# Optimization experiments

Hardware: AMD Instinct MI355X
Metric: run time of the kernel (lower is better)

## Reference

```python
import jax, jax.numpy as jnp
import numpy as np

B, S, E = 2, 2048, 1024
H, KV, D = 16, 4, 64
GC = 128          # ve_gate_channels
EPS = 1.1920929e-07  # torch F.rms_norm default eps for fp32
NEG = -1e30


def setup_inputs() -> dict:
    key = jax.random.key(0)
    ks = jax.random.split(key, 8)
    x = jax.random.normal(ks[0], (B, S, E), jnp.float32)
    ve = jax.random.normal(ks[1], (B, S, KV * D), jnp.float32)
    half = D // 2
    inv_freq = 1.0 / (10000.0 ** (np.arange(half, dtype=np.float64) / half))
    ang = np.arange(S, dtype=np.float64)[:, None] * inv_freq[None, :]
    cos = jnp.asarray(np.cos(ang), jnp.float32)[:, None, :]  # [S,1,D/2]
    sin = jnp.asarray(np.sin(ang), jnp.float32)[:, None, :]
    sc = E ** -0.5
    Wq = jax.random.normal(ks[2], (E, H * D), jnp.float32) * sc
    Wk = jax.random.normal(ks[3], (E, KV * D), jnp.float32) * sc
    Wv = jax.random.normal(ks[4], (E, KV * D), jnp.float32) * sc
    Wproj = jax.random.normal(ks[5], (E, E), jnp.float32) * sc
    Wgate = jax.random.normal(ks[6], (GC, KV), jnp.float32) * (GC ** -0.5)
    return {"x": x, "ve": ve, "cos": cos, "sin": sin, "Wq": Wq, "Wk": Wk,
            "Wv": Wv, "Wproj": Wproj, "Wgate": Wgate,
            "window_left": 1024, "window_right": 0}


def _rms(x):
    return x * jax.lax.rsqrt(jnp.mean(x * x, axis=-1, keepdims=True) + EPS)


def _rope(x, cos, sin):
    d = x.shape[-1] // 2
    x1, x2 = x[..., :d], x[..., d:]
    return jnp.concatenate([x1 * cos + x2 * sin, -x1 * sin + x2 * cos], axis=-1)


def reference(x, ve, cos, sin, Wq, Wk, Wv, Wproj, Wgate, window_left, window_right):
    b, s, e = x.shape
    q = (x @ Wq).reshape(b, s, H, D)
    k = (x @ Wk).reshape(b, s, KV, D)
    v = (x @ Wv).reshape(b, s, KV, D)
    # value-embedding gate: 2*sigmoid over first GC channels, per kv-head
    gate = 2.0 * jax.nn.sigmoid(x[..., :GC] @ Wgate)          # [B,S,KV]
    v = v + gate[..., None] * ve.reshape(b, s, KV, D)
    q = _rms(_rope(q, cos, sin))
    k = _rms(_rope(k, cos, sin))
    # GQA: repeat kv heads to match query heads
    g = H // KV
    kk = jnp.repeat(k, g, axis=2)                             # [B,S,H,D]
    vv = jnp.repeat(v, g, axis=2)
    scores = jnp.einsum('bihd,bjhd->bhij', q, kk) * (D ** -0.5)
    i = jnp.arange(s)[:, None]
    j = jnp.arange(s)[None, :]
    mask = (j <= i + window_right) & (j >= i - window_left) & (j <= i)
    scores = jnp.where(mask, scores, NEG)
    p = jax.nn.softmax(scores, axis=-1)
    y = jnp.einsum('bhij,bjhd->bihd', p, vv).reshape(b, s, H * D)
    return y @ Wproj
```

## Files before the change

kernel.cpp:

```cpp
#include <hip/hip_runtime.h>

typedef __bf16 bf16;
typedef __bf16 bf16x4 __attribute__((ext_vector_type(4)));
typedef __bf16 bf16x8 __attribute__((ext_vector_type(8)));
typedef float floatx4 __attribute__((ext_vector_type(4)));

#define EPS 1.1920929e-07f
#define QSCALE (0.125f * 1.44269504088896f)
#define SHIFT_C 11.5416f

__device__ __forceinline__ floatx4 mfma16(bf16x8 a, bf16x8 b, floatx4 c) {
  return __builtin_amdgcn_mfma_f32_16x16x32_bf16(a, b, c, 0, 0, 0);
}

__device__ __forceinline__ void gload16(const void* g, void* l) {
  __builtin_amdgcn_global_load_lds((const __attribute__((address_space(1))) unsigned int*)g,
                                   (__attribute__((address_space(3))) unsigned int*)l, 16, 0, 0);
}

__global__ void prep_kernel(const float* __restrict__ x, const float* __restrict__ wgate,
                            const float* __restrict__ Wq, const float* __restrict__ Wk,
                            const float* __restrict__ Wv, const float* __restrict__ Wproj,
                            bf16* __restrict__ xb, float* __restrict__ gate,
                            bf16* __restrict__ out_qkv, bf16* __restrict__ out_proj) {
  __shared__ float tile[32][33];
  const int tid = threadIdx.x;
  if (blockIdx.x < 4096) {
    int t = blockIdx.x;
    const float* xr = x + (size_t)t * 1024;
    float4 v = *(const float4*)(xr + tid * 4);
    bf16x4 o = {(bf16)v.x, (bf16)v.y, (bf16)v.z, (bf16)v.w};
    *(bf16x4*)(xb + (size_t)t * 1024 + tid * 4) = o;
    if (tid < 64) {
      int c = (tid & 31) * 4;
#pragma unroll
      for (int kv = 0; kv < 4; kv++) {
        float g = v.x * wgate[(c + 0) * 4 + kv] + v.y * wgate[(c + 1) * 4 + kv] +
                  v.z * wgate[(c + 2) * 4 + kv] + v.w * wgate[(c + 3) * 4 + kv];
        g += __shfl_xor(g, 1, 64);
        g += __shfl_xor(g, 2, 64);
        g += __shfl_xor(g, 4, 64);
        g += __shfl_xor(g, 8, 64);
        g += __shfl_xor(g, 16, 64);
        if (tid == 0) {
          int b = t >> 11, s = t & 2047;
          gate[((size_t)b * 4 + kv) * 2048 + s] = 2.f / (1.f + __expf(-g));
        }
      }
    }
  } else {
    int j = blockIdx.x - 4096;
    int ky = j / 80;
    int nx = j - ky * 80;
    int k0 = ky * 32;
    int tx = tid & 31, ty = tid >> 5;
    if (nx < 48) {
      int n0 = nx * 32;
#pragma unroll
      for (int i = 0; i < 4; i++) {
        int k = k0 + ty + i * 8, n = n0 + tx;
        float v;
        if (n < 1024)      v = Wq[(size_t)k * 1024 + n];
        else if (n < 1280) v = Wk[(size_t)k * 256 + (n - 1024)];
        else               v = Wv[(size_t)k * 256 + (n - 1280)];
        tile[ty + i * 8][tx] = v;
      }
      __syncthreads();
#pragma unroll
      for (int i = 0; i < 4; i++) {
        int n = n0 + ty + i * 8, k = k0 + tx;
        out_qkv[(size_t)n * 1024 + k] = (bf16)tile[tx][ty + i * 8];
      }
    } else {
      int n0 = (nx - 48) * 32;
#pragma unroll
      for (int i = 0; i < 4; i++)
        tile[ty + i * 8][tx] = Wproj[(size_t)(k0 + ty + i * 8) * 1024 + n0 + tx];
      __syncthreads();
#pragma unroll
      for (int i = 0; i < 4; i++)
        out_proj[(size_t)(n0 + ty + i * 8) * 1024 + k0 + tx] = (bf16)tile[tx][ty + i * 8];
    }
  }
}

__global__ __launch_bounds__(256) void qkv_gemm_kernel(const bf16* __restrict__ A,
                                                       const bf16* __restrict__ Bt,
                                                       const float* __restrict__ ve,
                                                       const float* __restrict__ cosb,
                                                       const float* __restrict__ sinb,
                                                       const float* __restrict__ gate,
                                                       bf16* __restrict__ Qb,
                                                       bf16* __restrict__ Kf,
                                                       bf16* __restrict__ Vf) {
  __shared__ __align__(16) char smem[24576];
  bf16* As = (bf16*)smem;
  bf16* Bs = (bf16*)(smem + 16384);
  bf16* Ep = (bf16*)smem;
  const int K = 1024;
  const int tid = threadIdx.x;
  const int orig = blockIdx.x;
  const int lid = (orig & 7) * 96 + (orig >> 3);
  const int tile = lid % 24;
  const int m0 = (lid / 24) * 128, n0 = tile * 64;
  const int w = tid >> 6, lane = tid & 63;
  const int q = lane >> 4, r0 = lane & 15;
  const int lrow = lane >> 2, lcol = (lane & 3) * 8;
  const int b = m0 >> 11, s0 = m0 & 2047;

  floatx4 acc[2][4];
#pragma unroll
  for (int i = 0; i < 2; i++)
#pragma unroll
    for (int j = 0; j < 4; j++) acc[i][j] = (floatx4){0.f, 0.f, 0.f, 0.f};

  for (int k0 = 0; k0 < K; k0 += 64) {
    __syncthreads();
#pragma unroll
    for (int i = 0; i < 4; i++) {
      int g = w * 4 + i, s = g >> 3, rb = g & 7;
      gload16(A + (size_t)(m0 + rb * 16 + lrow) * K + k0 + s * 32 + lcol, &As[s * 4096 + rb * 512]);
    }
#pragma unroll
    for (int i = 0; i < 2; i++) {
      int g = w * 2 + i, s = g >> 2, rb = g & 3;
      gload16(Bt + (size_t)(n0 + rb * 16 + lrow) * K + k0 + s * 32 + lcol, &Bs[s * 2048 + rb * 512]);
    }
    __syncthreads();
#pragma unroll
    for (int s = 0; s < 2; s++) {
      bf16x8 af[2], bfr[4];
#pragma unroll
      for (int mt = 0; mt < 2; mt++) af[mt] = *(const bf16x8*)&As[s * 4096 + (w * 32 + mt * 16 + r0) * 32 + q * 8];
#pragma unroll
      for (int nt = 0; nt < 4; nt++) bfr[nt] = *(const bf16x8*)&Bs[s * 2048 + (nt * 16 + r0) * 32 + q * 8];
#pragma unroll
      for (int mt = 0; mt < 2; mt++)
#pragma unroll
        for (int nt = 0; nt < 4; nt++)
          acc[mt][nt] = mfma16(af[mt], bfr[nt], acc[mt][nt]);
    }
  }
  __syncthreads();

  if (tile < 16) {
    const int h = tile;
#pragma unroll
    for (int mt = 0; mt < 2; mt++) {
      float rvv[4][4];
#pragma unroll
      for (int ntp = 0; ntp < 2; ntp++) {
        int d31 = ntp * 16 + r0;
#pragma unroll
        for (int r = 0; r < 4; r++) {
          int s = s0 + w * 32 + mt * 16 + q * 4 + r;
          float c = cosb[s * 32 + d31], sn = sinb[s * 32 + d31];
          float v1 = acc[mt][ntp][r], v2 = acc[mt][ntp + 2][r];
          rvv[ntp][r] = v1 * c + v2 * sn;
          rvv[ntp + 2][r] = v2 * c - v1 * sn;
        }
      }
#pragma unroll
      for (int r = 0; r < 4; r++) {
        float ss = 0.f;
#pragma unroll
        for (int nt = 0; nt < 4; nt++) ss += rvv[nt][r] * rvv[nt][r];
        ss += __shfl_xor(ss, 1, 64);
        ss += __shfl_xor(ss, 2, 64);
        ss += __shfl_xor(ss, 4, 64);
        ss += __shfl_xor(ss, 8, 64);
        float sc = rsqrtf(ss * (1.f / 64.f) + EPS) * QSCALE;
        int row = w * 32 + mt * 16 + q * 4 + r;
#pragma unroll
        for (int nt = 0; nt < 4; nt++)
          Ep[row * 72 + nt * 16 + r0] = (bf16)(rvv[nt][r] * sc);
      }
    }
    __syncthreads();
#pragma unroll
    for (int p = 0; p < 4; p++) {
      int g = p * 256 + tid;
      int row = g >> 3, chunk = g & 7;
      *(uint4*)&Qb[(((size_t)b * 16 + h) * 2048 + s0 + row) * 64 + chunk * 8] =
          *(const uint4*)&Ep[row * 72 + chunk * 8];
    }
  } else if (tile < 20) {
    const int kv = tile - 16;
#pragma unroll
    for (int mt = 0; mt < 2; mt++) {
      float rvv[4][4];
#pragma unroll
      for (int ntp = 0; ntp < 2; ntp++) {
        int d31 = ntp * 16 + r0;
#pragma unroll
        for (int r = 0; r < 4; r++) {
          int s = s0 + w * 32 + mt * 16 + q * 4 + r;
          float c = cosb[s * 32 + d31], sn = sinb[s * 32 + d31];
          float v1 = acc[mt][ntp][r], v2 = acc[mt][ntp + 2][r];
          rvv[ntp][r] = v1 * c + v2 * sn;
          rvv[ntp + 2][r] = v2 * c - v1 * sn;
        }
      }
#pragma unroll
      for (int r = 0; r < 4; r++) {
        float ss = 0.f;
#pragma unroll
        for (int nt = 0; nt < 4; nt++) ss += rvv[nt][r] * rvv[nt][r];
        ss += __shfl_xor(ss, 1, 64);
        ss += __shfl_xor(ss, 2, 64);
        ss += __shfl_xor(ss, 4, 64);
        ss += __shfl_xor(ss, 8, 64);
        float sc = rsqrtf(ss * (1.f / 64.f) + EPS);
        int row = w * 32 + mt * 16 + q * 4 + r;
#pragma unroll
        for (int nt = 0; nt < 4; nt++)
          Ep[row * 72 + nt * 16 + r0] = (bf16)(rvv[nt][r] * sc);
      }
    }
    __syncthreads();
    {
      int tk = (s0 >> 5) + w;
      size_t tb = ((size_t)(b * 4 + kv) * 64 + tk) * 2048;
#pragma unroll
      for (int u = 0; u < 4; u++) {
        int joff = (u >= 2) ? 16 : 0, doff = (u & 1) * 32;
        bf16x8 f = *(const bf16x8*)&Ep[(w * 32 + joff + r0) * 72 + doff + q * 8];
        *(bf16x8*)&Kf[tb + u * 512 + lane * 8] = f;
      }
    }
  } else {
    const int kv = tile - 20;
    const float* gbase = gate + ((size_t)b * 4 + kv) * 2048;
#pragma unroll
    for (int mt = 0; mt < 2; mt++) {
#pragma unroll
      for (int r = 0; r < 4; r++) {
        int row = w * 32 + mt * 16 + q * 4 + r;
        float gg = gbase[s0 + row];
#pragma unroll
        for (int nt = 0; nt < 4; nt++) {
          int d = nt * 16 + r0;
          float vv = acc[mt][nt][r] + gg * ve[(size_t)(m0 + row) * 256 + kv * 64 + d];
          Ep[row * 72 + d] = (bf16)vv;
        }
      }
    }
    __syncthreads();
    {
      int tk = (s0 >> 5) + w;
      size_t tb = ((size_t)(b * 4 + kv) * 64 + tk) * 2048;
#pragma unroll
      for (int nt = 0; nt < 4; nt++) {
        bf16 tmp[8];
#pragma unroll
        for (int e = 0; e < 8; e++) {
          int jl = w * 32 + (e >> 2) * 16 + 4 * q + (e & 3);
          tmp[e] = Ep[jl * 72 + nt * 16 + r0];
        }
        *(uint4*)&Vf[tb + nt * 512 + lane * 8] = *(uint4*)tmp;
      }
    }
  }
}

__global__ __launch_bounds__(256) void proj_gemm_kernel(const bf16* __restrict__ A,
                                                        const bf16* __restrict__ Bt,
                                                        float* __restrict__ Cout) {
  __shared__ __align__(16) bf16 As[2 * 128 * 32];
  __shared__ __align__(16) bf16 Bs[2 * 64 * 32];
  const int K = 1024, N = 1024;
  const int tid = threadIdx.x;
  const int orig = blockIdx.x;
  const int lid = (orig & 7) * 64 + (orig >> 3);
  const int m0 = (lid / 16) * 128, n0 = (lid % 16) * 64;
  const int w = tid >> 6, lane = tid & 63;
  const int q = lane >> 4, r0 = lane & 15;
  const int lrow = lane >> 2, lcol = (lane & 3) * 8;

  floatx4 acc[2][4];
#pragma unroll
  for (int i = 0; i < 2; i++)
#pragma unroll
    for (int j = 0; j < 4; j++) acc[i][j] = (floatx4){0.f, 0.f, 0.f, 0.f};

  for (int k0 = 0; k0 < K; k0 += 64) {
    __syncthreads();
#pragma unroll
    for (int i = 0; i < 4; i++) {
      int g = w * 4 + i, s = g >> 3, rb = g & 7;
      gload16(A + (size_t)(m0 + rb * 16 + lrow) * K + k0 + s * 32 + lcol, &As[s * 4096 + rb * 512]);
    }
#pragma unroll
    for (int i = 0; i < 2; i++) {
      int g = w * 2 + i, s = g >> 2, rb = g & 3;
      gload16(Bt + (size_t)(n0 + rb * 16 + lrow) * K + k0 + s * 32 + lcol, &Bs[s * 2048 + rb * 512]);
    }
    __syncthreads();
#pragma unroll
    for (int s = 0; s < 2; s++) {
      bf16x8 af[2], bfr[4];
#pragma unroll
      for (int mt = 0; mt < 2; mt++) af[mt] = *(const bf16x8*)&As[s * 4096 + (w * 32 + mt * 16 + r0) * 32 + q * 8];
#pragma unroll
      for (int nt = 0; nt < 4; nt++) bfr[nt] = *(const bf16x8*)&Bs[s * 2048 + (nt * 16 + r0) * 32 + q * 8];
#pragma unroll
      for (int mt = 0; mt < 2; mt++)
#pragma unroll
        for (int nt = 0; nt < 4; nt++)
          acc[mt][nt] = mfma16(af[mt], bfr[nt], acc[mt][nt]);
    }
  }
#pragma unroll
  for (int mt = 0; mt < 2; mt++)
#pragma unroll
    for (int nt = 0; nt < 4; nt++)
#pragma unroll
      for (int r = 0; r < 4; r++) {
        int row = m0 + w * 32 + mt * 16 + q * 4 + r;
        int col = n0 + nt * 16 + r0;
        Cout[(size_t)row * N + col] = acc[mt][nt][r];
      }
}

__global__ __launch_bounds__(256, 4) void attn_kernel(const bf16* __restrict__ Qb,
                                                      const bf16* __restrict__ Kf,
                                                      const bf16* __restrict__ Vf,
                                                      const int* __restrict__ wlp,
                                                      const int* __restrict__ wrp,
                                                      bf16* __restrict__ Yb) {
  __shared__ __align__(16) bf16 Ks[2048];
  __shared__ __align__(16) bf16 Vs[2048];
  const int wl = wlp[0];
  const int wrc = min(wrp[0], 0);
  const int blk = blockIdx.x;
  const int bkv = blk & 7;
  const int b = bkv >> 2, kvh = bkv & 3;
  const int cm = 127 - (blk >> 3);
  const int w = threadIdx.x >> 6, lane = threadIdx.x & 63;
  const int q = lane >> 4, r0 = lane & 15;
  const int h = kvh * 4 + w;
  const int q0 = cm << 4;

  const bf16* qbase = Qb + (((size_t)b * 16 + h) * 2048 + q0 + r0) * 64;
  bf16x8 aq0 = *(const bf16x8*)(qbase + q * 8);
  bf16x8 aq1 = *(const bf16x8*)(qbase + 32 + q * 8);

  floatx4 O[4];
#pragma unroll
  for (int nt = 0; nt < 4; nt++) O[nt] = (floatx4){0.f, 0.f, 0.f, 0.f};
  floatx4 L = (floatx4){0.f, 0.f, 0.f, 0.f};

  const bf16 onev = (bf16)1.0f;
  const bf16x8 ones = {onev, onev, onev, onev, onev, onev, onev, onev};

  const int jlo = max(0, q0 - wl) & ~31;
  const int jhi = q0 + 15 + wrc;
  const int count = ((jhi - jlo) >> 5) + 1;
  const int tile0 = jlo >> 5;

  const bf16* kfb = Kf + ((size_t)(b * 4 + kvh) * 64) * 2048;
  const bf16* vfb = Vf + ((size_t)(b * 4 + kvh) * 64) * 2048;

  for (int t = 0; t < count; t++) {
    const int j0 = jlo + (t << 5);
    const bf16* kt = kfb + (size_t)(tile0 + t) * 2048;
    const bf16* vt = vfb + (size_t)(tile0 + t) * 2048;
    __syncthreads();
#pragma unroll
    for (int i = 0; i < 2; i++) {
      int c = 2 * w + i;
      if (c < 4) gload16(kt + c * 512 + lane * 8, &Ks[c * 512]);
      else       gload16(vt + (c - 4) * 512 + lane * 8, &Vs[(c - 4) * 512]);
    }
    __syncthreads();

    bf16x8 kf0 = *(const bf16x8*)&Ks[0 * 512 + lane * 8];
    bf16x8 kf1 = *(const bf16x8*)&Ks[1 * 512 + lane * 8];
    bf16x8 kf2 = *(const bf16x8*)&Ks[2 * 512 + lane * 8];
    bf16x8 kf3 = *(const bf16x8*)&Ks[3 * 512 + lane * 8];

    floatx4 s0 = (floatx4){-SHIFT_C, -SHIFT_C, -SHIFT_C, -SHIFT_C};
    floatx4 s1 = s0;
    __builtin_amdgcn_s_setprio(1);
    s0 = mfma16(kf0, aq0, s0);
    s0 = mfma16(kf1, aq1, s0);
    s1 = mfma16(kf2, aq0, s1);
    s1 = mfma16(kf3, aq1, s1);
    __builtin_amdgcn_s_setprio(0);

    bf16x8 pa;
    if (j0 >= q0 + 15 - wl && j0 + 31 <= q0 + wrc) {
#pragma unroll
      for (int r = 0; r < 4; r++) {
        pa[r] = (bf16)exp2f(s0[r]);
        pa[4 + r] = (bf16)exp2f(s1[r]);
      }
    } else {
      const int i = q0 + r0;
#pragma unroll
      for (int r = 0; r < 4; r++) {
        int ja = j0 + 4 * q + r, jb = ja + 16;
        bool va = (ja <= i + wrc) && (ja >= i - wl);
        bool vb = (jb <= i + wrc) && (jb >= i - wl);
        pa[r] = va ? (bf16)exp2f(s0[r]) : (bf16)0.f;
        pa[4 + r] = vb ? (bf16)exp2f(s1[r]) : (bf16)0.f;
      }
    }

    bf16x8 vf0 = *(const bf16x8*)&Vs[0 * 512 + lane * 8];
    bf16x8 vf1 = *(const bf16x8*)&Vs[1 * 512 + lane * 8];
    bf16x8 vf2 = *(const bf16x8*)&Vs[2 * 512 + lane * 8];
    bf16x8 vf3 = *(const bf16x8*)&Vs[3 * 512 + lane * 8];

    __builtin_amdgcn_s_setprio(1);
    L = mfma16(pa, ones, L);
    O[0] = mfma16(pa, vf0, O[0]);
    O[1] = mfma16(pa, vf1, O[1]);
    O[2] = mfma16(pa, vf2, O[2]);
    O[3] = mfma16(pa, vf3, O[3]);
    __builtin_amdgcn_s_setprio(0);
  }

  float inv[4];
#pragma unroll
  for (int r = 0; r < 4; r++) inv[r] = 1.f / L[r];
#pragma unroll
  for (int nt = 0; nt < 4; nt++)
#pragma unroll
    for (int r = 0; r < 4; r++) {
      int i = q0 + q * 4 + r;
      Yb[((size_t)b * 2048 + i) * 1024 + h * 64 + nt * 16 + r0] = (bf16)(O[nt][r] * inv[r]);
    }
}

extern "C" void kernel_launch(void* const* d_in, const int* in_sizes, int n_in,
                              void* d_out, int out_size, void* d_ws, size_t ws_size,
                              hipStream_t stream) {
  const float* x     = (const float*)d_in[0];
  const float* ve    = (const float*)d_in[1];
  const float* cosb  = (const float*)d_in[2];
  const float* sinb  = (const float*)d_in[3];
  const float* Wq    = (const float*)d_in[4];
  const float* Wk    = (const float*)d_in[5];
  const float* Wv    = (const float*)d_in[6];
  const float* Wproj = (const float*)d_in[7];
  const float* Wgate = (const float*)d_in[8];
  const int* wl      = (const int*)d_in[9];
  const int* wr      = (const int*)d_in[10];

  char* ws = (char*)d_ws;
  bf16* Xb      = (bf16*)(ws);
  bf16* Wqkv_t  = (bf16*)(ws + 8388608);
  bf16* Wproj_t = (bf16*)(ws + 11534336);
  bf16* Qb      = (bf16*)(ws + 13631488);
  bf16* Kf      = (bf16*)(ws + 22020096);
  bf16* Vf      = (bf16*)(ws + 24117248);
  bf16* Yb      = (bf16*)(ws + 26214400);
  float* gateb  = (float*)(ws + 34603008);

  prep_kernel<<<4096 + 2560, 256, 0, stream>>>(x, Wgate, Wq, Wk, Wv, Wproj, Xb, gateb, Wqkv_t, Wproj_t);
  qkv_gemm_kernel<<<768, 256, 0, stream>>>(Xb, Wqkv_t, ve, cosb, sinb, gateb, Qb, Kf, Vf);
  attn_kernel<<<1024, 256, 0, stream>>>(Qb, Kf, Vf, wl, wr, Yb);
  proj_gemm_kernel<<<512, 256, 0, stream>>>(Yb, Wproj_t, (float*)d_out);
}
```

Before: 163.3 us.

## Process two 16-row query tiles per attention block to reuse K/V tiles

Each attention block now handles 32 query rows (two 16-row sub-tiles) instead of 16, so every K/V tile loaded into shared memory feeds twice as many MFMAs. The grid is halved to 512 blocks and the occupancy hint is dropped from launch_bounds. The aim is to cut global/LDS load traffic and barrier overhead per unit of work. The cost is more registers per thread and fewer blocks, which can lower occupancy and latency hiding. Each block also walks one extra key tile at the diagonal.

```diff
diff --git a/kernel.cpp b/kernel.cpp
--- a/kernel.cpp
+++ b/kernel.cpp
@@ -322,12 +322,12 @@
       }
 }
 
-__global__ __launch_bounds__(256, 4) void attn_kernel(const bf16* __restrict__ Qb,
-                                                      const bf16* __restrict__ Kf,
-                                                      const bf16* __restrict__ Vf,
-                                                      const int* __restrict__ wlp,
-                                                      const int* __restrict__ wrp,
-                                                      bf16* __restrict__ Yb) {
+__global__ __launch_bounds__(256) void attn_kernel(const bf16* __restrict__ Qb,
+                                                   const bf16* __restrict__ Kf,
+                                                   const bf16* __restrict__ Vf,
+                                                   const int* __restrict__ wlp,
+                                                   const int* __restrict__ wrp,
+                                                   bf16* __restrict__ Yb) {
   __shared__ __align__(16) bf16 Ks[2048];
   __shared__ __align__(16) bf16 Vs[2048];
   const int wl = wlp[0];
@@ -335,26 +335,33 @@
   const int blk = blockIdx.x;
   const int bkv = blk & 7;
   const int b = bkv >> 2, kvh = bkv & 3;
-  const int cm = 127 - (blk >> 3);
+  const int cm = 63 - (blk >> 3);
   const int w = threadIdx.x >> 6, lane = threadIdx.x & 63;
   const int q = lane >> 4, r0 = lane & 15;
   const int h = kvh * 4 + w;
-  const int q0 = cm << 4;
-
-  const bf16* qbase = Qb + (((size_t)b * 16 + h) * 2048 + q0 + r0) * 64;
-  bf16x8 aq0 = *(const bf16x8*)(qbase + q * 8);
-  bf16x8 aq1 = *(const bf16x8*)(qbase + 32 + q * 8);
-
-  floatx4 O[4];
-#pragma unroll
-  for (int nt = 0; nt < 4; nt++) O[nt] = (floatx4){0.f, 0.f, 0.f, 0.f};
-  floatx4 L = (floatx4){0.f, 0.f, 0.f, 0.f};
+  const int q0 = cm << 5;
+  const int qA = q0, qB = q0 + 16;
+
+  const bf16* qbase = Qb + (((size_t)b * 16 + h) * 2048 + qA + r0) * 64;
+  bf16x8 aqA0 = *(const bf16x8*)(qbase + q * 8);
+  bf16x8 aqA1 = *(const bf16x8*)(qbase + 32 + q * 8);
+  bf16x8 aqB0 = *(const bf16x8*)(qbase + 16 * 64 + q * 8);
+  bf16x8 aqB1 = *(const bf16x8*)(qbase + 16 * 64 + 32 + q * 8);
+
+  floatx4 OA[4], OB[4];
+#pragma unroll
+  for (int nt = 0; nt < 4; nt++) {
+    OA[nt] = (floatx4){0.f, 0.f, 0.f, 0.f};
+    OB[nt] = (floatx4){0.f, 0.f, 0.f, 0.f};
+  }
+  floatx4 LA = (floatx4){0.f, 0.f, 0.f, 0.f};
+  floatx4 LB = LA;
 
   const bf16 onev = (bf16)1.0f;
   const bf16x8 ones = {onev, onev, onev, onev, onev, onev, onev, onev};
 
   const int jlo = max(0, q0 - wl) & ~31;
-  const int jhi = q0 + 15 + wrc;
+  const int jhi = q0 + 31 + wrc;
   const int count = ((jhi - jlo) >> 5) + 1;
   const int tile0 = jlo >> 5;
 
@@ -379,31 +386,52 @@
     bf16x8 kf2 = *(const bf16x8*)&Ks[2 * 512 + lane * 8];
     bf16x8 kf3 = *(const bf16x8*)&Ks[3 * 512 + lane * 8];
 
-    floatx4 s0 = (floatx4){-SHIFT_C, -SHIFT_C, -SHIFT_C, -SHIFT_C};
-    floatx4 s1 = s0;
+    floatx4 sA0 = (floatx4){-SHIFT_C, -SHIFT_C, -SHIFT_C, -SHIFT_C};
+    floatx4 sA1 = sA0, sB0 = sA0, sB1 = sA0;
     __builtin_amdgcn_s_setprio(1);
-    s0 = mfma16(kf0, aq0, s0);
-    s0 = mfma16(kf1, aq1, s0);
-    s1 = mfma16(kf2, aq0, s1);
-    s1 = mfma16(kf3, aq1, s1);
+    sA0 = mfma16(kf0, aqA0, sA0);
+    sA0 = mfma16(kf1, aqA1, sA0);
+    sA1 = mfma16(kf2, aqA0, sA1);
+    sA1 = mfma16(kf3, aqA1, sA1);
+    sB0 = mfma16(kf0, aqB0, sB0);
+    sB0 = mfma16(kf1, aqB1, sB0);
+    sB1 = mfma16(kf2, aqB0, sB1);
+    sB1 = mfma16(kf3, aqB1, sB1);
     __builtin_amdgcn_s_setprio(0);
 
-    bf16x8 pa;
-    if (j0 >= q0 + 15 - wl && j0 + 31 <= q0 + wrc) {
-#pragma unroll
-      for (int r = 0; r < 4; r++) {
-        pa[r] = (bf16)exp2f(s0[r]);
-        pa[4 + r] = (bf16)exp2f(s1[r]);
+    bf16x8 paA, paB;
+    if (j0 >= qA + 15 - wl && j0 + 31 <= qA + wrc) {
+#pragma unroll
+      for (int r = 0; r < 4; r++) {
+        paA[r] = (bf16)exp2f(sA0[r]);
+        paA[4 + r] = (bf16)exp2f(sA1[r]);
       }
     } else {
-      const int i = q0 + r0;
+      const int i = qA + r0;
 #pragma unroll
       for (int r = 0; r < 4; r++) {
         int ja = j0 + 4 * q + r, jb = ja + 16;
         bool va = (ja <= i + wrc) && (ja >= i - wl);
         bool vb = (jb <= i + wrc) && (jb >= i - wl);
-        pa[r] = va ? (bf16)exp2f(s0[r]) : (bf16)0.f;
-        pa[4 + r] = vb ? (bf16)exp2f(s1[r]) : (bf16)0.f;
+        paA[r] = va ? (bf16)exp2f(sA0[r]) : (bf16)0.f;
+        paA[4 + r] = vb ? (bf16)exp2f(sA1[r]) : (bf16)0.f;
+      }
+    }
+    if (j0 >= qB + 15 - wl && j0 + 31 <= qB + wrc) {
+#pragma unroll
+      for (int r = 0; r < 4; r++) {
+        paB[r] = (bf16)exp2f(sB0[r]);
+        paB[4 + r] = (bf16)exp2f(sB1[r]);
+      }
+    } else {
+      const int i = qB + r0;
+#pragma unroll
+      for (int r = 0; r < 4; r++) {
+        int ja = j0 + 4 * q + r, jb = ja + 16;
+        bool va = (ja <= i + wrc) && (ja >= i - wl);
+        bool vb = (jb <= i + wrc) && (jb >= i - wl);
+        paB[r] = va ? (bf16)exp2f(sB0[r]) : (bf16)0.f;
+        paB[4 + r] = vb ? (bf16)exp2f(sB1[r]) : (bf16)0.f;
       }
     }
 
@@ -413,23 +441,33 @@
     bf16x8 vf3 = *(const bf16x8*)&Vs[3 * 512 + lane * 8];
 
     __builtin_amdgcn_s_setprio(1);
-    L = mfma16(pa, ones, L);
-    O[0] = mfma16(pa, vf0, O[0]);
-    O[1] = mfma16(pa, vf1, O[1]);
-    O[2] = mfma16(pa, vf2, O[2]);
-    O[3] = mfma16(pa, vf3, O[3]);
+    LA = mfma16(paA, ones, LA);
+    LB = mfma16(paB, ones, LB);
+    OA[0] = mfma16(paA, vf0, OA[0]);
+    OA[1] = mfma16(paA, vf1, OA[1]);
+    OA[2] = mfma16(paA, vf2, OA[2]);
+    OA[3] = mfma16(paA, vf3, OA[3]);
+    OB[0] = mfma16(paB, vf0, OB[0]);
+    OB[1] = mfma16(paB, vf1, OB[1]);
+    OB[2] = mfma16(paB, vf2, OB[2]);
+    OB[3] = mfma16(paB, vf3, OB[3]);
     __builtin_amdgcn_s_setprio(0);
   }
 
-  float inv[4];
-#pragma unroll
-  for (int r = 0; r < 4; r++) inv[r] = 1.f / L[r];
+  float invA[4], invB[4];
+#pragma unroll
+  for (int r = 0; r < 4; r++) {
+    invA[r] = 1.f / LA[r];
+    invB[r] = 1.f / LB[r];
+  }
 #pragma unroll
   for (int nt = 0; nt < 4; nt++)
 #pragma unroll
     for (int r = 0; r < 4; r++) {
-      int i = q0 + q * 4 + r;
-      Yb[((size_t)b * 2048 + i) * 1024 + h * 64 + nt * 16 + r0] = (bf16)(O[nt][r] * inv[r]);
+      int iA = qA + q * 4 + r;
+      Yb[((size_t)b * 2048 + iA) * 1024 + h * 64 + nt * 16 + r0] = (bf16)(OA[nt][r] * invA[r]);
+      int iB = qB + q * 4 + r;
+      Yb[((size_t)b * 2048 + iB) * 1024 + h * 64 + nt * 16 + r0] = (bf16)(OB[nt][r] * invB[r]);
     }
 }
 
@@ -460,6 +498,6 @@
 
   prep_kernel<<<4096 + 2560, 256, 0, stream>>>(x, Wgate, Wq, Wk, Wv, Wproj, Xb, gateb, Wqkv_t, Wproj_t);
   qkv_gemm_kernel<<<768, 256, 0, stream>>>(Xb, Wqkv_t, ve, cosb, sinb, gateb, Qb, Kf, Vf);
-  attn_kernel<<<1024, 256, 0, stream>>>(Qb, Kf, Vf, wl, wr, Yb);
+  attn_kernel<<<512, 256, 0, stream>>>(Qb, Kf, Vf, wl, wr, Yb);
   proj_gemm_kernel<<<512, 256, 0, stream>>>(Yb, Wproj_t, (float*)d_out);
 }
```

Result: slower. 172.2 us (+5.4%).
